# Kernel tuning notes

Hardware: AMD Instinct MI355X
Metric: run time of the kernel (lower is better)

## Reference

```python
import jax, jax.numpy as jnp
import numpy as np

LMAX = 8                         # lmax-1 used by s2/so3 irreps
DIMS = [2 * l + 1 for l in range(LMAX + 1)]
S2_OFF = np.cumsum([0] + DIMS).tolist()            # offsets into 81-dim s2 irreps
SO3_OFF = np.cumsum([0] + [d * d for d in DIMS]).tolist()  # offsets into 969-dim so3 irreps
S2_DIM = S2_OFF[-1]              # 81
SO3_DIM = SO3_OFF[-1]            # 969
F_IN = 81                        # multiplicity into S2Conv
F_SO3 = 300
C = 768                          # encoder feature channels
KS = 7                           # encoder feature map / kernel size
B = 8
G_S2 = 48                        # s2 healpix grid rec_level=1
G_ACT = 4096                     # SO3Activation grid points (stand-in for res=20 grid)
G_SO3 = 36864                    # so3 healpix grid rec_level=3


def setup_inputs() -> dict:
    key = jax.random.key(0)
    ks = jax.random.split(key, 7)
    return {
        "x": jax.random.normal(ks[0], (B, C, KS, KS), jnp.float32),
        "F": jax.random.normal(ks[1], (F_IN, S2_DIM * C, KS, KS), jnp.float32) * 0.02,
        "w_s2": jax.random.normal(ks[2], (F_IN, F_SO3, G_S2), jnp.float32) * 0.1,
        "Y": jax.random.normal(ks[3], (G_S2, S2_DIM), jnp.float32),
        "w_so3": jax.random.normal(ks[4], (F_SO3, 1, G_SO3), jnp.float32) * 0.1,
        "D": jax.random.normal(ks[5], (G_SO3, SO3_DIM), jnp.float32),
        "D_act": jax.random.normal(ks[6], (G_ACT, SO3_DIM), jnp.float32),
    }


def _forward(x, F, w_s2, Y, w_so3, D, D_act):
    b = x.shape[0]
    # ---- Induction layer: split expanded R2Conv filter into 768-channel chunks,
    # stack, contract with feature map. g_split: (n=81, c_out=81, C, 7, 7)
    g = jnp.swapaxes(F.reshape(F_IN, S2_DIM, C, KS, KS), 0, 1)
    y = jnp.einsum('ijkhw,akhw->aji', g, x)          # (B, 81, 81): (batch, f_in, s2 irreps)

    # ---- S2Conv: expand kernel into irrep space, per-l block linear (s2 -> so3 irreps)
    psi = jnp.einsum('ni,xyn->xyi', Y, w_s2) / np.sqrt(G_S2)  # (81, 300, 81)
    outs = []
    for l, d in enumerate(DIMS):
        o = S2_OFF[l]
        xl = y[:, :, o:o + d]                        # (B, f_in, 2l+1)
        wl = psi[:, :, o:o + d]                      # (f_in, f_out, mul_out=2l+1)
        ol = jnp.einsum('bfm,fgu->bgum', xl, wl) / np.sqrt(F_IN)
        outs.append(ol.reshape(b, F_SO3, d * d))
    z = jnp.concatenate(outs, axis=-1)               # (B, 300, 969)

    # ---- SO3Activation: to grid, relu, back to irreps
    s = jnp.einsum('bfi,gi->bfg', z, D_act)
    z = jnp.einsum('bfg,gi->bfi', jax.nn.relu(s), D_act) / G_ACT

    # ---- SO3Conv: expand kernel via Wigner-D buffer, per-l block linear (so3 -> so3)
    psi2 = jnp.einsum('ni,xyn->xyi', D, w_so3) / np.sqrt(G_SO3)  # (300, 1, 969)
    outs = []
    for l, d in enumerate(DIMS):
        o = SO3_OFF[l]
        xl = z[:, :, o:o + d * d].reshape(b, F_SO3, d, d)   # (B, f, u, m)
        wl = psi2[:, :, o:o + d * d].reshape(F_SO3, 1, d, d)  # (f, g, v, u)
        ol = jnp.einsum('bfum,fgvu->bgvm', xl, wl) / np.sqrt(F_SO3 * d)
        outs.append(ol.reshape(b, 1, d * d))
    return jnp.concatenate(outs, axis=-1)            # (B, 1, 969)


def reference(x, F, w_s2, Y, w_so3, D, D_act):
    return _forward(x, F, w_s2, Y, w_so3, D, D_act)
```

## Files before the change

kernel.cpp:

```cpp
#include <hip/hip_runtime.h>
#include <hip/hip_bf16.h>
#include <math.h>

#define THREADS 256

constexpr int B_    = 8;
constexpr int C_    = 768;
constexpr int KS_   = 7;
constexpr int F_IN  = 81;
constexpr int F_SO3 = 300;
constexpr int S2_DIM  = 81;
constexpr int SO3_DIM = 969;
constexpr int G_S2  = 48;
constexpr int G_ACT = 4096;
constexpr int G_SO3 = 36864;
constexpr int CKK   = C_ * KS_ * KS_;
constexpr int CKK4  = CKK / 4;
constexpr int NPAIR = F_IN * S2_DIM;

constexpr int D2_SPLIT = 4;
constexpr int E1_SPLIT = 16;
constexpr int F_SPLIT  = 5;

__constant__ int d_S2_OFF[10]  = {0, 1, 4, 9, 16, 25, 36, 49, 64, 81};
__constant__ int d_SO3_OFF[10] = {0, 1, 10, 35, 84, 165, 286, 455, 680, 969};

struct CEnt { unsigned char u, m, so, l; };
struct CLut { CEnt v[992]; };
constexpr CLut make_clut() {
  CLut t{};
  int S2O[10]  = {0, 1, 4, 9, 16, 25, 36, 49, 64, 81};
  int SO3O[10] = {0, 1, 10, 35, 84, 165, 286, 455, 680, 969};
  for (int i = 0; i < 969; ++i) {
    int l = 0;
    while (i >= SO3O[l + 1]) ++l;
    int d = 2 * l + 1, r = i - SO3O[l];
    t.v[i].u  = (unsigned char)(r / d);
    t.v[i].m  = (unsigned char)(r % d);
    t.v[i].so = (unsigned char)S2O[l];
    t.v[i].l  = (unsigned char)l;
  }
  return t;
}
__constant__ CLut g_clut = make_clut();

using short8 = __attribute__((ext_vector_type(8))) short;
using f32x4  = __attribute__((ext_vector_type(4))) float;
using f4v    = __attribute__((ext_vector_type(4))) float;

#define GL16(gp, lp)                                                        \
  __builtin_amdgcn_global_load_lds(                                         \
      (const __attribute__((address_space(1))) void*)(gp),                  \
      (__attribute__((address_space(3))) void*)(lp), 16, 0, 0)

#define WAIT_VMCNT6() asm volatile("s_waitcnt vmcnt(6)" ::: "memory")
#define BARRIER()                                   \
  do {                                              \
    __builtin_amdgcn_sched_barrier(0);              \
    __builtin_amdgcn_s_barrier();                   \
    __builtin_amdgcn_sched_barrier(0);              \
  } while (0)

constexpr size_t AL(size_t x) { return (x + 1023) & ~(size_t)1023; }
constexpr size_t O_Y     = 0;
constexpr size_t O_PSI   = O_Y     + AL((size_t)8 * NPAIR * 4);
constexpr size_t O_ZBF   = O_PSI   + AL((size_t)F_IN * F_SO3 * 81 * 4);
constexpr size_t O_DACT  = O_ZBF   + AL((size_t)2432 * 1024 * 2);
constexpr size_t O_DACTT = O_DACT  + AL((size_t)4096 * 1024 * 2);
constexpr size_t O_WSO3  = O_DACTT + AL((size_t)1024 * 4096 * 2);
constexpr size_t O_DT    = O_WSO3  + AL((size_t)384 * 36864 * 2);
constexpr size_t O_SBF   = O_DT    + AL((size_t)1024 * 36864 * 2);
constexpr size_t O_D2P   = O_SBF   + AL((size_t)2432 * 4096 * 2);
constexpr size_t O_E1P   = O_D2P   + AL((size_t)D2_SPLIT * 2432 * 1024 * 4);
constexpr size_t O_PSI2  = O_E1P   + AL((size_t)E1_SPLIT * 384 * 1024 * 4);
constexpr size_t O_SFP   = O_PSI2  + AL((size_t)F_SO3 * SO3_DIM * 4);
constexpr size_t FAST_NEED = O_SFP + AL((size_t)F_SPLIT * 8 * SO3_DIM * 4);

constexpr size_t WS_Y    = 0;
constexpr size_t WS_PSI  = 52488;
constexpr size_t WS_Z    = 2020788;
constexpr size_t WS_S    = 4346388;
constexpr size_t WS_Z2   = 14176788;
constexpr size_t WS_P2P  = 16502388;
constexpr size_t WS_PSI2 = 18827988;

__device__ __forceinline__ void stage_a_body(
    const float* __restrict__ Fm, const float* __restrict__ x, float* __restrict__ y,
    char* smemc, int blk) {
  const int p0  = blk * 3;
  const int tid = threadIdx.x;
  const f4v* __restrict__ F4 = (const f4v*)Fm;
  const f4v* __restrict__ x4 = (const f4v*)x;

  float acc[3][8];
#pragma unroll
  for (int p = 0; p < 3; ++p)
#pragma unroll
    for (int b = 0; b < 8; ++b) acc[p][b] = 0.f;

  for (int i = tid; i < CKK4; i += THREADS) {
    f4v xv[8];
#pragma unroll
    for (int b = 0; b < 8; ++b) xv[b] = x4[b * CKK4 + i];
#pragma unroll
    for (int p = 0; p < 3; ++p) {
      f4v fv = __builtin_nontemporal_load(&F4[(size_t)(p0 + p) * CKK4 + i]);
#pragma unroll
      for (int b = 0; b < 8; ++b)
        acc[p][b] += fv[0] * xv[b][0] + fv[1] * xv[b][1] + fv[2] * xv[b][2] + fv[3] * xv[b][3];
    }
  }

  float (*red)[24] = (float(*)[24])smemc;
  const int lane = tid & 63, wid = tid >> 6;
#pragma unroll
  for (int p = 0; p < 3; ++p) {
#pragma unroll
    for (int b = 0; b < 8; ++b) {
      float v = acc[p][b];
      v += __shfl_down(v, 32);
      v += __shfl_down(v, 16);
      v += __shfl_down(v, 8);
      v += __shfl_down(v, 4);
      v += __shfl_down(v, 2);
      v += __shfl_down(v, 1);
      if (lane == 0) red[wid][p * 8 + b] = v;
    }
  }
  __syncthreads();
  if (tid < 24) {
    float v = red[0][tid] + red[1][tid] + red[2][tid] + red[3][tid];
    int p = tid / 8, b = tid % 8;
    y[(size_t)b * NPAIR + p0 + p] = v;
  }
}

__global__ __launch_bounds__(THREADS) void k_stage_a3(
    const float* __restrict__ Fm, const float* __restrict__ x, float* __restrict__ y) {
  __shared__ __align__(16) char smem[512];
  stage_a_body(Fm, x, y, smem, blockIdx.x);
}

__device__ __forceinline__ void cvt4_body(const float* __restrict__ src,
                                          __hip_bfloat16* __restrict__ dst,
                                          int R, int Cs, int Cp, int blk) {
  size_t e0 = ((size_t)blk * THREADS + threadIdx.x) * 4;
  int r = (int)(e0 / (unsigned)Cp), c = (int)(e0 % (unsigned)Cp);
  __hip_bfloat16 o[4];
#pragma unroll
  for (int j = 0; j < 4; ++j) {
    float v = (r < R && c + j < Cs) ? src[(size_t)r * Cs + c + j] : 0.f;
    o[j] = __float2bfloat16(v);
  }
  *(ushort4*)(&dst[e0]) = *(const ushort4*)o;
}

__device__ __forceinline__ void tr_body(const float* __restrict__ src,
                                        __hip_bfloat16* __restrict__ dst,
                                        int R, int Cs, size_t dstStride, int bx, int by,
                                        char* smemc) {
  float (*tile)[33] = (float(*)[33])smemc;
  const int c0 = bx * 32, r0 = by * 32;
  const int tx = threadIdx.x & 31, ty = threadIdx.x >> 5;
#pragma unroll
  for (int i = 0; i < 32; i += 8) {
    int r = r0 + ty + i, c = c0 + tx;
    tile[ty + i][tx] = (c < Cs) ? src[(size_t)r * Cs + c] : 0.f;
  }
  __syncthreads();
  const int rp = threadIdx.x & 15;
  const int cl = threadIdx.x >> 4;
#pragma unroll
  for (int j = 0; j < 2; ++j) {
    int cc = cl + 16 * j;
    int c  = c0 + cc;
    if (c < Cs) {
      __hip_bfloat16 o[2];
      o[0] = __float2bfloat16(tile[2 * rp][cc]);
      o[1] = __float2bfloat16(tile[2 * rp + 1][cc]);
      *(ushort2*)(&dst[(size_t)c * dstStride + r0 + 2 * rp]) = *(const ushort2*)o;
    }
  }
}

__device__ __forceinline__ void psi_body(const float* __restrict__ w_s2,
                                         const float* __restrict__ Y,
                                         float* __restrict__ psi_t, int blk) {
  int idx = blk * THREADS + threadIdx.x;
  if (idx >= F_IN * F_SO3 * S2_DIM) return;
  int s  = idx % S2_DIM;
  int t1 = idx / S2_DIM;
  int f  = t1 % F_IN;
  int g  = t1 / F_IN;
  const float* w = w_s2 + ((size_t)f * F_SO3 + g) * G_S2;
  float acc = 0.f;
#pragma unroll 8
  for (int n = 0; n < G_S2; ++n) acc += w[n] * Y[n * S2_DIM + s];
  psi_t[idx] = acc * 0.14433756729740643f;
}

constexpr int UB1 = 4096;
constexpr int UB2 = 3968;
constexpr int UB3 = 13824;
constexpr int UB4 = 35712;
constexpr int UB5 = 7689;
constexpr int UB_TOT = UB1 + UB2 + UB3 + UB4 + UB5;

__global__ __launch_bounds__(THREADS) void k_uber(
    const float* __restrict__ D_act, __hip_bfloat16* __restrict__ Dact_bf,
    __hip_bfloat16* __restrict__ DactT_bf,
    const float* __restrict__ w_so3, __hip_bfloat16* __restrict__ wso3_bf,
    const float* __restrict__ D, __hip_bfloat16* __restrict__ DT_bf,
    const float* __restrict__ w_s2, const float* __restrict__ Y, float* __restrict__ psi_t) {
  __shared__ __align__(16) char smem[4352];
  int b = blockIdx.x;
  if (b < UB1) { cvt4_body(D_act, Dact_bf, G_ACT, SO3_DIM, 1024, b); return; }
  b -= UB1;
  if (b < UB2) { tr_body(D_act, DactT_bf, G_ACT, SO3_DIM, 4096, b % 31, b / 31, smem); return; }
  b -= UB2;
  if (b < UB3) { cvt4_body(w_so3, wso3_bf, F_SO3, G_SO3, G_SO3, b); return; }
  b -= UB3;
  if (b < UB4) { tr_body(D, DT_bf, G_SO3, SO3_DIM, 36864, b % 31, b / 31, smem); return; }
  b -= UB4;
  psi_body(w_s2, Y, psi_t, b);
}

__global__ __launch_bounds__(THREADS) void k_stage_c_bf(
    const float* __restrict__ y, const float* __restrict__ psi_t,
    __hip_bfloat16* __restrict__ z) {
  const int b = blockIdx.x / F_SO3;
  const int g = blockIdx.x % F_SO3;
  __shared__ float ybl[NPAIR];
  __shared__ float psl[NPAIR];
  const int tid = threadIdx.x;
  const float* pg = psi_t + (size_t)g * NPAIR;
  for (int t = tid; t < NPAIR; t += THREADS) {
    ybl[t] = y[(size_t)b * NPAIR + t];
    psl[t] = pg[t];
  }
  __syncthreads();
  for (int i = tid; i < 1024; i += THREADS) {
    float acc = 0.f;
    if (i < SO3_DIM) {
      CEnt e = g_clut.v[i];
      int im = e.so + e.m, iu = e.so + e.u;
#pragma unroll 9
      for (int f = 0; f < F_IN; ++f)
        acc += ybl[f * S2_DIM + im] * psl[f * S2_DIM + iu];
      acc *= (1.0f / 9.0f);
    }
    z[((size_t)b * F_SO3 + g) * 1024 + i] = __float2bfloat16(acc);
  }
}

struct G256 {
  const __hip_bfloat16* A;
  const __hip_bfloat16* B;
  void* C;
  int K, kSpan, Ncols;
  float scale;
  size_t splitStride;
  int gx, gy, gz, epi;
};

__device__ __forceinline__ void mfma256_body(const G256& g, unsigned lin, char* smem) {
  unsigned nwg = (unsigned)(g.gx * g.gy * g.gz);
  if ((nwg & 7u) == 0u) {
    unsigned q = nwg >> 3;
    lin = (lin & 7u) * q + (lin >> 3);
  }
  const int bxi = (int)(lin % (unsigned)g.gx);
  const unsigned t1 = lin / (unsigned)g.gx;
  const int byi = (int)(t1 % (unsigned)g.gy);
  const int bzi = (int)(t1 / (unsigned)g.gy);

  const int t    = threadIdx.x;
  const int lane = t & 63;
  const int wid  = t >> 6;
  const int wr   = wid >> 2, wc = wid & 3;
  const int bm = byi * 128, bn = bxi * 256;
  const int kBegin = bzi * g.kSpan;
  const int NG = g.kSpan >> 6;

  int aL[2], bL[4];
  const char* aSrc[2];
  const char* bSrc[4];
#pragma unroll
  for (int i = 0; i < 2; ++i) {
    int L = (i * 512 + t) * 16;
    int row = L >> 7;
    int kb  = (L & 127) ^ ((row & 7) << 4);
    aL[i] = L;
    aSrc[i] = (const char*)g.A + ((size_t)(bm + row) * g.K) * 2 + kb;
  }
#pragma unroll
  for (int i = 0; i < 4; ++i) {
    int L = (i * 512 + t) * 16;
    int row = L >> 7;
    int kb  = (L & 127) ^ ((row & 7) << 4);
    bL[i] = L;
    bSrc[i] = (const char*)g.B + ((size_t)(bn + row) * g.K) * 2 + kb;
  }

  auto STAGE = [&](int buf, int kt) {
    size_t ko = (size_t)(kBegin + (kt << 6)) * 2;
    char* Ab = smem + buf * 49152;
    char* Bb = Ab + 16384;
#pragma unroll
    for (int i = 0; i < 2; ++i) GL16(aSrc[i] + ko, Ab + aL[i]);
#pragma unroll
    for (int i = 0; i < 4; ++i) GL16(bSrc[i] + ko, Bb + bL[i]);
  };

  f32x4 acc[4][4] = {};

  STAGE(0, 0);
  STAGE(1, 1);
  WAIT_VMCNT6();
  BARRIER();

  int bi = 0;
  for (int gg = 0; gg < NG; ++gg) {
    char* Ab = smem + bi * 49152;
    char* Bb = Ab + 16384;
    short8 af[2][4], bf[2][4];

#pragma unroll
    for (int kk = 0; kk < 2; ++kk) {
      const int klin = (kk << 6) + ((lane >> 4) << 4);
#pragma unroll
      for (int m = 0; m < 4; ++m) {
        int ra = (wr << 6) + (m << 4) + (lane & 15);
        af[kk][m] = *(const short8*)(Ab + ra * 128 + (klin ^ ((ra & 7) << 4)));
      }
#pragma unroll
      for (int n = 0; n < 4; ++n) {
        int rb = (wc << 6) + (n << 4) + (lane & 15);
        bf[kk][n] = *(const short8*)(Bb + rb * 128 + (klin ^ ((rb & 7) << 4)));
      }
    }
    {
      int b2 = bi + 2; if (b2 >= 3) b2 -= 3;
      int kt2 = (gg + 2 < NG) ? gg + 2 : 0;
      STAGE(b2, kt2);
    }
    WAIT_VMCNT6();
    BARRIER();
    __builtin_amdgcn_s_setprio(1);
#pragma unroll
    for (int kk = 0; kk < 2; ++kk)
#pragma unroll
      for (int m = 0; m < 4; ++m)
#pragma unroll
        for (int n = 0; n < 4; ++n)
          acc[m][n] = __builtin_amdgcn_mfma_f32_16x16x32_bf16(af[kk][m], bf[kk][n], acc[m][n], 0, 0, 0);
    __builtin_amdgcn_s_setprio(0);
    BARRIER();

    if (++bi == 3) bi = 0;
  }

  const int rbase = bm + (wr << 6) + ((lane >> 4) << 2);
  const int cbase = bn + (wc << 6) + (lane & 15);
  if (g.epi == 0) {
    float* C = (float*)g.C + (size_t)bzi * g.splitStride;
#pragma unroll
    for (int m = 0; m < 4; ++m)
#pragma unroll
      for (int n = 0; n < 4; ++n)
#pragma unroll
        for (int r = 0; r < 4; ++r)
          C[(size_t)(rbase + m * 16 + r) * g.Ncols + (cbase + n * 16)] = acc[m][n][r] * g.scale;
  } else {
    __hip_bfloat16* C = (__hip_bfloat16*)g.C;
#pragma unroll
    for (int m = 0; m < 4; ++m)
#pragma unroll
      for (int n = 0; n < 4; ++n)
#pragma unroll
        for (int r = 0; r < 4; ++r)
          C[(size_t)(rbase + m * 16 + r) * g.Ncols + (cbase + n * 16)] =
              __float2bfloat16(fmaxf(acc[m][n][r], 0.f));
  }
}

__global__ __launch_bounds__(512) void k_g256_dual(G256 g0, G256 g1, int n0) {
  __shared__ __align__(16) char smem[147456];
  if ((int)blockIdx.x < n0) mfma256_body(g0, blockIdx.x, smem);
  else                      mfma256_body(g1, blockIdx.x - n0, smem);
}

__global__ __launch_bounds__(512) void k_g256_d2_e1r(
    G256 g, int n0,
    const float* __restrict__ parts, float* __restrict__ psi2) {
  __shared__ __align__(16) char smem[147456];
  if ((int)blockIdx.x < n0) { mfma256_body(g, blockIdx.x, smem); return; }
  int idx = (int)(blockIdx.x - n0) * 512 + threadIdx.x;
  if (idx >= F_SO3 * SO3_DIM) return;
  int r = idx / SO3_DIM, c = idx % SO3_DIM;
  float a = 0.f;
#pragma unroll
  for (int s = 0; s < E1_SPLIT; ++s) a += parts[(size_t)s * (384 * 1024) + (size_t)r * 1024 + c];
  psi2[(size_t)r * SO3_DIM + c] = a * (1.0f / 192.0f);
}

__global__ __launch_bounds__(THREADS) void k_stage_f_part(
    const float* __restrict__ d2p, const float* __restrict__ psi2, float* __restrict__ partial) {
  const int b  = blockIdx.x / 9;
  const int l  = blockIdx.x % 9;
  const int sp = blockIdx.y;
  const int d = 2 * l + 1, d2 = d * d;
  const int off = d_SO3_OFF[l];
  constexpr size_t SS = (size_t)2432 * 1024;
  __shared__ float zb[10][289];
  __shared__ float pb[10][289];
  const int tid = threadIdx.x;
  float acc[2] = {0.f, 0.f};
  const int fBeg = sp * (F_SO3 / F_SPLIT), fEnd = fBeg + F_SO3 / F_SPLIT;
  for (int fc = fBeg; fc < fEnd; fc += 10) {
    for (int t = tid; t < 10 * d2; t += THREADS) {
      int fl = t / d2, q = t - fl * d2;
      int f  = fc + fl;
      size_t zi = ((size_t)b * F_SO3 + f) * 1024 + off + q;
      float zv = 0.f;
#pragma unroll
      for (int s = 0; s < D2_SPLIT; ++s) zv += d2p[zi + (size_t)s * SS];
      zb[fl][q] = zv * (1.0f / G_ACT);
      pb[fl][q] = psi2[(size_t)f * SO3_DIM + off + q];
    }
    __syncthreads();
#pragma unroll 2
    for (int io = 0; io < 2; ++io) {
      int i = tid + io * THREADS;
      if (i < d2) {
        int v = i / d, m = i - v * d;
        float a = acc[io];
#pragma unroll
        for (int fl = 0; fl < 10; ++fl) {
          float s_ = 0.f;
          for (int u = 0; u < d; ++u)
            s_ += zb[fl][u * d + m] * pb[fl][v * d + u];
          a += s_;
        }
        acc[io] = a;
      }
    }
    __syncthreads();
  }
  for (int io = 0; io < 2; ++io) {
    int i = tid + io * THREADS;
    if (i < d2) partial[((size_t)sp * 8 + b) * SO3_DIM + off + i] = acc[io];
  }
}

__global__ __launch_bounds__(THREADS) void k_stage_f_red(
    const float* __restrict__ partial, float* __restrict__ out) {
  int idx = blockIdx.x * THREADS + threadIdx.x;
  if (idx >= 8 * SO3_DIM) return;
  int b = idx / SO3_DIM, i = idx % SO3_DIM;
  int l = g_clut.v[i].l;
  float a = 0.f;
#pragma unroll
  for (int sp = 0; sp < F_SPLIT; ++sp)
    a += partial[((size_t)sp * 8 + b) * SO3_DIM + i];
  out[(size_t)b * SO3_DIM + i] = a * rsqrtf(300.0f * (float)(2 * l + 1));
}

__global__ __launch_bounds__(THREADS) void k_psi(
    const float* __restrict__ w_s2, const float* __restrict__ Y, float* __restrict__ psi_t) {
  psi_body(w_s2, Y, psi_t, blockIdx.x);
}

__global__ __launch_bounds__(THREADS) void k_stage_c(
    const float* __restrict__ y, const float* __restrict__ psi_t, float* __restrict__ z) {
  const int b = blockIdx.x / F_SO3;
  const int g = blockIdx.x % F_SO3;
  __shared__ float ybl[NPAIR];
  __shared__ float psl[NPAIR];
  const int tid = threadIdx.x;
  const float* pg = psi_t + (size_t)g * NPAIR;
  for (int t = tid; t < NPAIR; t += THREADS) {
    ybl[t] = y[(size_t)b * NPAIR + t];
    psl[t] = pg[t];
  }
  __syncthreads();
  for (int i = tid; i < SO3_DIM; i += THREADS) {
    CEnt e = g_clut.v[i];
    int im = e.so + e.m, iu = e.so + e.u;
    float acc = 0.f;
#pragma unroll 9
    for (int f = 0; f < F_IN; ++f)
      acc += ybl[f * S2_DIM + im] * psl[f * S2_DIM + iu];
    z[((size_t)b * F_SO3 + g) * SO3_DIM + i] = acc * (1.0f / 9.0f);
  }
}

__global__ __launch_bounds__(THREADS) void k_gemm_nt_relu(
    const float* __restrict__ A, const float* __restrict__ Bm, float* __restrict__ Cm,
    int M, int N, int K) {
  __shared__ float As[16][68];
  __shared__ float Bs[16][68];
  const int bm = blockIdx.y * 64, bn = blockIdx.x * 64;
  const int t  = threadIdx.x;
  const int lk = t & 15, lm = t >> 4;
  const int tn = t & 15, tm = t >> 4;
  float acc[4][4] = {};
  for (int k0 = 0; k0 < K; k0 += 16) {
    int gk = k0 + lk;
#pragma unroll
    for (int j = 0; j < 4; ++j) {
      int m  = lm + 16 * j;
      int gm = bm + m;
      As[lk][m] = (gm < M && gk < K) ? A[(size_t)gm * K + gk] : 0.f;
      int gn = bn + m;
      Bs[lk][m] = (gn < N && gk < K) ? Bm[(size_t)gn * K + gk] : 0.f;
    }
    __syncthreads();
#pragma unroll
    for (int k = 0; k < 16; ++k) {
      float4 av = *(const float4*)&As[k][tm * 4];
      float4 bv = *(const float4*)&Bs[k][tn * 4];
      float a[4] = {av.x, av.y, av.z, av.w};
      float bb[4] = {bv.x, bv.y, bv.z, bv.w};
#pragma unroll
      for (int i2 = 0; i2 < 4; ++i2)
#pragma unroll
        for (int j2 = 0; j2 < 4; ++j2)
          acc[i2][j2] += a[i2] * bb[j2];
    }
    __syncthreads();
  }
#pragma unroll
  for (int i2 = 0; i2 < 4; ++i2) {
    int gm = bm + tm * 4 + i2;
    if (gm >= M) continue;
#pragma unroll
    for (int j2 = 0; j2 < 4; ++j2) {
      int gn = bn + tn * 4 + j2;
      if (gn < N) Cm[(size_t)gm * N + gn] = fmaxf(acc[i2][j2], 0.f);
    }
  }
}

__global__ __launch_bounds__(THREADS) void k_gemm_nn(
    const float* __restrict__ A, const float* __restrict__ Bm, float* __restrict__ Cm,
    int M, int N, int K, int kSpan, float scale, size_t cStride) {
  __shared__ float As[16][68];
  __shared__ float Bs[16][68];
  const int bm = blockIdx.y * 64, bn = blockIdx.x * 64;
  const int t   = threadIdx.x;
  const int lk  = t & 15, lm = t >> 4;
  const int ln  = t & 63, lkq = t >> 6;
  const int tn  = t & 15, tm = t >> 4;
  const int kBegin = blockIdx.z * kSpan;
  const int kEnd   = kBegin + kSpan;
  float* C = Cm + (size_t)blockIdx.z * cStride;
  float acc[4][4] = {};
  for (int k0 = kBegin; k0 < kEnd; k0 += 16) {
    {
      int gk = k0 + lk;
#pragma unroll
      for (int j = 0; j < 4; ++j) {
        int m = lm + 16 * j, gm = bm + m;
        As[lk][m] = (gm < M) ? A[(size_t)gm * K + gk] : 0.f;
      }
    }
    {
      int gn = bn + ln;
#pragma unroll
      for (int j = 0; j < 4; ++j) {
        int k = lkq + 4 * j;
        Bs[k][ln] = (gn < N) ? Bm[(size_t)(k0 + k) * N + gn] : 0.f;
      }
    }
    __syncthreads();
#pragma unroll
    for (int k = 0; k < 16; ++k) {
      float4 av = *(const float4*)&As[k][tm * 4];
      float4 bv = *(const float4*)&Bs[k][tn * 4];
      float a[4] = {av.x, av.y, av.z, av.w};
      float bb[4] = {bv.x, bv.y, bv.z, bv.w};
#pragma unroll
      for (int i2 = 0; i2 < 4; ++i2)
#pragma unroll
        for (int j2 = 0; j2 < 4; ++j2)
          acc[i2][j2] += a[i2] * bb[j2];
    }
    __syncthreads();
  }
#pragma unroll
  for (int i2 = 0; i2 < 4; ++i2) {
    int gm = bm + tm * 4 + i2;
    if (gm >= M) continue;
#pragma unroll
    for (int j2 = 0; j2 < 4; ++j2) {
      int gn = bn + tn * 4 + j2;
      if (gn < N) C[(size_t)gm * N + gn] = acc[i2][j2] * scale;
    }
  }
}

__global__ __launch_bounds__(THREADS) void k_reduce_psi2(
    const float* __restrict__ parts, float* __restrict__ psi2) {
  int idx = blockIdx.x * THREADS + threadIdx.x;
  if (idx >= F_SO3 * SO3_DIM) return;
  float acc = 0.f;
#pragma unroll
  for (int s = 0; s < 8; ++s) acc += parts[(size_t)s * (F_SO3 * SO3_DIM) + idx];
  psi2[idx] = acc * (1.0f / 192.0f);
}

__global__ __launch_bounds__(THREADS) void k_stage_f(
    const float* __restrict__ z2, const float* __restrict__ psi2, float* __restrict__ out,
    int zStride) {
  const int b = blockIdx.x / 9;
  const int l = blockIdx.x % 9;
  const int d = 2 * l + 1, d2 = d * d;
  const int off = d_SO3_OFF[l];
  __shared__ float zb[10][289];
  __shared__ float pb[10][289];
  const int tid = threadIdx.x;
  float acc[2] = {0.f, 0.f};
  const float scale = rsqrtf(300.0f * (float)d);
  for (int fc = 0; fc < F_SO3; fc += 10) {
    for (int t = tid; t < 10 * d2; t += THREADS) {
      int fl = t / d2, q = t - fl * d2;
      int f  = fc + fl;
      zb[fl][q] = z2[((size_t)b * F_SO3 + f) * zStride + off + q];
      pb[fl][q] = psi2[(size_t)f * SO3_DIM + off + q];
    }
    __syncthreads();
#pragma unroll 2
    for (int io = 0; io < 2; ++io) {
      int i = tid + io * THREADS;
      if (i < d2) {
        int v = i / d, m = i - v * d;
        float a = acc[io];
#pragma unroll
        for (int fl = 0; fl < 10; ++fl) {
          float s_ = 0.f;
          for (int u = 0; u < d; ++u)
            s_ += zb[fl][u * d + m] * pb[fl][v * d + u];
          a += s_;
        }
        acc[io] = a;
      }
    }
    __syncthreads();
  }
  for (int io = 0; io < 2; ++io) {
    int i = tid + io * THREADS;
    if (i < d2) out[(size_t)b * SO3_DIM + off + i] = acc[io] * scale;
  }
}

extern "C" void kernel_launch(void* const* d_in, const int* in_sizes, int n_in,
                              void* d_out, int out_size, void* d_ws, size_t ws_size,
                              hipStream_t stream) {
  const float* x     = (const float*)d_in[0];
  const float* Fm    = (const float*)d_in[1];
  const float* w_s2  = (const float*)d_in[2];
  const float* Y     = (const float*)d_in[3];
  const float* w_so3 = (const float*)d_in[4];
  const float* D     = (const float*)d_in[5];
  const float* D_act = (const float*)d_in[6];
  float* out = (float*)d_out;

  if (ws_size >= FAST_NEED) {
    char* p = (char*)d_ws;
    float*          y       = (float*)(p + O_Y);
    float*          psi     = (float*)(p + O_PSI);
    __hip_bfloat16* z_bf    = (__hip_bfloat16*)(p + O_ZBF);
    __hip_bfloat16* Dact_bf = (__hip_bfloat16*)(p + O_DACT);
    __hip_bfloat16* DactT_bf= (__hip_bfloat16*)(p + O_DACTT);
    __hip_bfloat16* wso3_bf = (__hip_bfloat16*)(p + O_WSO3);
    __hip_bfloat16* DT_bf   = (__hip_bfloat16*)(p + O_DT);
    __hip_bfloat16* s_bf    = (__hip_bfloat16*)(p + O_SBF);
    float*          d2p     = (float*)(p + O_D2P);
    float*          e1p     = (float*)(p + O_E1P);
    float*          psi2    = (float*)(p + O_PSI2);
    float*          sfp     = (float*)(p + O_SFP);

    k_stage_a3<<<NPAIR / 3, THREADS, 0, stream>>>(Fm, x, y);
    k_uber<<<UB_TOT, THREADS, 0, stream>>>(
        D_act, Dact_bf, DactT_bf, w_so3, wso3_bf, D, DT_bf, w_s2, Y, psi);
    k_stage_c_bf<<<B_ * F_SO3, THREADS, 0, stream>>>(y, psi, z_bf);

    G256 e1{wso3_bf, DT_bf, e1p, G_SO3, G_SO3 / E1_SPLIT, 1024, 1.f,
            (size_t)384 * 1024, 4, 3, E1_SPLIT, 0};
    G256 d1{z_bf, Dact_bf, s_bf, 1024, 1024, 4096, 1.f, 0, 16, 19, 1, 1};
    int nE1 = 4 * 3 * E1_SPLIT;
    int nD1 = 16 * 19;
    k_g256_dual<<<nE1 + nD1, 512, 0, stream>>>(e1, d1, nE1);

    G256 d2{s_bf, DactT_bf, d2p, 4096, 4096 / D2_SPLIT, 1024, 1.f,
            (size_t)2432 * 1024, 4, 19, D2_SPLIT, 0};
    int nD2  = 4 * 19 * D2_SPLIT;
    int nE1r = (F_SO3 * SO3_DIM + 511) / 512;
    k_g256_d2_e1r<<<nD2 + nE1r, 512, 0, stream>>>(d2, nD2, e1p, psi2);

    k_stage_f_part<<<dim3(B_ * 9, F_SPLIT), THREADS, 0, stream>>>(d2p, psi2, sfp);
    k_stage_f_red<<<(8 * SO3_DIM + THREADS - 1) / THREADS, THREADS, 0, stream>>>(sfp, out);
  } else {
    float* ws  = (float*)d_ws;
    float* y    = ws + WS_Y;
    float* psi  = ws + WS_PSI;
    float* z    = ws + WS_Z;
    float* s    = ws + WS_S;
    float* z2   = ws + WS_Z2;
    float* p2p  = ws + WS_P2P;
    float* psi2 = ws + WS_PSI2;

    k_stage_a3<<<NPAIR / 3, THREADS, 0, stream>>>(Fm, x, y);
    k_psi<<<(F_IN * F_SO3 * S2_DIM + THREADS - 1) / THREADS, THREADS, 0, stream>>>(w_s2, Y, psi);
    k_stage_c<<<B_ * F_SO3, THREADS, 0, stream>>>(y, psi, z);
    k_gemm_nt_relu<<<dim3(G_ACT / 64, (B_ * F_SO3 + 63) / 64), THREADS, 0, stream>>>(
        z, D_act, s, B_ * F_SO3, G_ACT, SO3_DIM);
    k_gemm_nn<<<dim3((SO3_DIM + 63) / 64, (B_ * F_SO3 + 63) / 64, 1), THREADS, 0, stream>>>(
        s, D_act, z2, B_ * F_SO3, SO3_DIM, G_ACT, G_ACT, 1.0f / G_ACT, 0);
    k_gemm_nn<<<dim3((SO3_DIM + 63) / 64, (F_SO3 + 63) / 64, 8), THREADS, 0, stream>>>(
        w_so3, D, p2p, F_SO3, SO3_DIM, G_SO3, G_SO3 / 8, 1.0f, (size_t)F_SO3 * SO3_DIM);
    k_reduce_psi2<<<(F_SO3 * SO3_DIM + THREADS - 1) / THREADS, THREADS, 0, stream>>>(p2p, psi2);
    k_stage_f<<<B_ * 9, THREADS, 0, stream>>>(z2, psi2, out, SO3_DIM);
  }
}
```

Before: 561.8 us.

## Stage MFMA epilogue through LDS for vector stores; register-block stage C

The GEMM epilogue now writes each wave's accumulator tile into a padded LDS staging area, then reads it back row-wise and issues 16-byte fp32 or 8-byte bf16 vector stores instead of scattered scalar stores. Separately, the S2Conv block-linear kernel is reorganized so each thread computes four consecutive m outputs for one (l,u) pair, reusing each psi value across four y reads, with padded LDS rows. This is meant to cut uncoalesced global writes and redundant LDS loads. It reuses the pipeline's shared memory for staging with no barrier before the overwrite, which could race with other waves, and the bf16 epilogue now multiplies by scale where it did not before.

```diff
diff --git a/kernel.cpp b/kernel.cpp
--- a/kernel.cpp
+++ b/kernel.cpp
@@ -43,6 +43,22 @@
   return t;
 }
 __constant__ CLut g_clut = make_clut();
+
+struct CItem { unsigned char l, u, m0; };
+struct CItems { CItem v[288]; };
+constexpr CItems make_citems() {
+  CItems t{};
+  int k = 0;
+  for (int l = 0; l < 9; ++l) {
+    int d = 2 * l + 1;
+    for (int u = 0; u < d; ++u)
+      for (int m0 = 0; m0 < d; m0 += 4)
+        t.v[k++] = {(unsigned char)l, (unsigned char)u, (unsigned char)m0};
+  }
+  return t;
+}
+__constant__ CItems g_citems = make_citems();
+constexpr int N_CITEMS = 285;
 
 using short8 = __attribute__((ext_vector_type(8))) short;
 using f32x4  = __attribute__((ext_vector_type(4))) float;
@@ -230,26 +246,48 @@
     __hip_bfloat16* __restrict__ z) {
   const int b = blockIdx.x / F_SO3;
   const int g = blockIdx.x % F_SO3;
-  __shared__ float ybl[NPAIR];
-  __shared__ float psl[NPAIR];
+  __shared__ float ybl[81 * 84];
+  __shared__ float psl[81 * 84];
   const int tid = threadIdx.x;
   const float* pg = psi_t + (size_t)g * NPAIR;
-  for (int t = tid; t < NPAIR; t += THREADS) {
-    ybl[t] = y[(size_t)b * NPAIR + t];
-    psl[t] = pg[t];
+  for (int idx = tid; idx < 81 * 84; idx += THREADS) {
+    int f = idx / 84, s = idx - f * 84;
+    float yv = 0.f, pv = 0.f;
+    if (s < 81) {
+      yv = y[(size_t)b * NPAIR + f * 81 + s];
+      pv = pg[f * 81 + s];
+    }
+    ybl[idx] = yv;
+    psl[idx] = pv;
   }
   __syncthreads();
-  for (int i = tid; i < 1024; i += THREADS) {
-    float acc = 0.f;
-    if (i < SO3_DIM) {
-      CEnt e = g_clut.v[i];
-      int im = e.so + e.m, iu = e.so + e.u;
-#pragma unroll 9
-      for (int f = 0; f < F_IN; ++f)
-        acc += ybl[f * S2_DIM + im] * psl[f * S2_DIM + iu];
-      acc *= (1.0f / 9.0f);
-    }
-    z[((size_t)b * F_SO3 + g) * 1024 + i] = __float2bfloat16(acc);
+
+  __hip_bfloat16* zrow = z + ((size_t)b * F_SO3 + g) * 1024;
+  if (tid < 1024 - 969) zrow[969 + tid] = __float2bfloat16(0.f);
+
+  for (int it = tid; it < N_CITEMS; it += THREADS) {
+    CItem e = g_citems.v[it];
+    const int d  = 2 * e.l + 1;
+    const int so = d_S2_OFF[e.l];
+    const int off = d_SO3_OFF[e.l];
+    const int base0 = so + e.m0;
+    const int pu = so + e.u;
+    float a0 = 0.f, a1 = 0.f, a2 = 0.f, a3 = 0.f;
+#pragma unroll 3
+    for (int f = 0; f < F_IN; ++f) {
+      const float* yb = &ybl[f * 84 + base0];
+      float pv = psl[f * 84 + pu];
+      a0 += pv * yb[0];
+      a1 += pv * yb[1];
+      a2 += pv * yb[2];
+      a3 += pv * yb[3];
+    }
+    int nm = d - e.m0;
+    size_t zo = (size_t)off + (size_t)e.u * d + e.m0;
+    zrow[zo] = __float2bfloat16(a0 * (1.0f / 9.0f));
+    if (nm > 1) zrow[zo + 1] = __float2bfloat16(a1 * (1.0f / 9.0f));
+    if (nm > 2) zrow[zo + 2] = __float2bfloat16(a2 * (1.0f / 9.0f));
+    if (nm > 3) zrow[zo + 3] = __float2bfloat16(a3 * (1.0f / 9.0f));
   }
 }
 
@@ -360,27 +398,39 @@
     if (++bi == 3) bi = 0;
   }
 
-  const int rbase = bm + (wr << 6) + ((lane >> 4) << 2);
-  const int cbase = bn + (wc << 6) + (lane & 15);
+  float* stg = (float*)(smem + wid * 17408);
+#pragma unroll
+  for (int m = 0; m < 4; ++m)
+#pragma unroll
+    for (int n = 0; n < 4; ++n)
+#pragma unroll
+      for (int r = 0; r < 4; ++r)
+        stg[(m * 16 + ((lane >> 4) << 2) + r) * 68 + n * 16 + (lane & 15)] = acc[m][n][r];
+
+  const int rowbase = bm + (wr << 6);
+  const int colbase = bn + (wc << 6);
   if (g.epi == 0) {
     float* C = (float*)g.C + (size_t)bzi * g.splitStride;
 #pragma unroll
-    for (int m = 0; m < 4; ++m)
-#pragma unroll
-      for (int n = 0; n < 4; ++n)
-#pragma unroll
-        for (int r = 0; r < 4; ++r)
-          C[(size_t)(rbase + m * 16 + r) * g.Ncols + (cbase + n * 16)] = acc[m][n][r] * g.scale;
+    for (int itv = 0; itv < 16; ++itv) {
+      int row  = itv * 4 + (lane >> 4);
+      int col4 = (lane & 15) * 4;
+      f4v v = *(const f4v*)&stg[row * 68 + col4];
+      f4v o = {v[0] * g.scale, v[1] * g.scale, v[2] * g.scale, v[3] * g.scale};
+      *(f4v*)&C[(size_t)(rowbase + row) * g.Ncols + colbase + col4] = o;
+    }
   } else {
     __hip_bfloat16* C = (__hip_bfloat16*)g.C;
 #pragma unroll
-    for (int m = 0; m < 4; ++m)
-#pragma unroll
-      for (int n = 0; n < 4; ++n)
-#pragma unroll
-        for (int r = 0; r < 4; ++r)
-          C[(size_t)(rbase + m * 16 + r) * g.Ncols + (cbase + n * 16)] =
-              __float2bfloat16(fmaxf(acc[m][n][r], 0.f));
+    for (int itv = 0; itv < 16; ++itv) {
+      int row  = itv * 4 + (lane >> 4);
+      int col4 = (lane & 15) * 4;
+      f4v v = *(const f4v*)&stg[row * 68 + col4];
+      __hip_bfloat16 o[4];
+#pragma unroll
+      for (int j = 0; j < 4; ++j) o[j] = __float2bfloat16(fmaxf(v[j] * g.scale, 0.f));
+      *(ushort4*)&C[(size_t)(rowbase + row) * g.Ncols + colbase + col4] = *(const ushort4*)o;
+    }
   }
 }
 
```

Result: slower. 594.2 us (+5.8%).

## Retile bf16 MFMA GEMMs to 128x128 tiles with 256-thread double buffering

Applied to the files above, without the earlier changes.

Replaces the 128x256, 512-thread, triple-buffered GEMM body with a 128x128 tile computed by 256 threads over two LDS buffers. Each buffer is refilled right after its fragments are read into registers, guarded by an lgkmcnt wait and a barrier. LDS per block drops from 144KB to 64KB, which should allow more resident blocks per CU, and the grids double in the N dimension. The K-split for the w_so3 x D GEMM rises from 16 to 24 to add more blocks, at the cost of more partial buffers to reduce. Smaller tiles lower data reuse per block, and the extra barrier per iteration adds synchronization.

```diff
diff --git a/kernel.cpp b/kernel.cpp
--- a/kernel.cpp
+++ b/kernel.cpp
@@ -19,7 +19,7 @@
 constexpr int NPAIR = F_IN * S2_DIM;
 
 constexpr int D2_SPLIT = 4;
-constexpr int E1_SPLIT = 16;
+constexpr int E1_SPLIT = 24;
 constexpr int F_SPLIT  = 5;
 
 __constant__ int d_S2_OFF[10]  = {0, 1, 4, 9, 16, 25, 36, 49, 64, 81};
@@ -53,7 +53,12 @@
       (const __attribute__((address_space(1))) void*)(gp),                  \
       (__attribute__((address_space(3))) void*)(lp), 16, 0, 0)
 
-#define WAIT_VMCNT6() asm volatile("s_waitcnt vmcnt(6)" ::: "memory")
+#define WAIT_VMCNT8() asm volatile("s_waitcnt vmcnt(8)" ::: "memory")
+#define LGKM0()                                     \
+  do {                                              \
+    asm volatile("s_waitcnt lgkmcnt(0)" ::: "memory"); \
+    __builtin_amdgcn_sched_barrier(0);              \
+  } while (0)
 #define BARRIER()                                   \
   do {                                              \
     __builtin_amdgcn_sched_barrier(0);              \
@@ -263,7 +268,7 @@
   int gx, gy, gz, epi;
 };
 
-__device__ __forceinline__ void mfma256_body(const G256& g, unsigned lin, char* smem) {
+__device__ __forceinline__ void mfma128_body(const G256& g, unsigned lin, char* smem) {
   unsigned nwg = (unsigned)(g.gx * g.gy * g.gz);
   if ((nwg & 7u) == 0u) {
     unsigned q = nwg >> 3;
@@ -277,37 +282,31 @@
   const int t    = threadIdx.x;
   const int lane = t & 63;
   const int wid  = t >> 6;
-  const int wr   = wid >> 2, wc = wid & 3;
-  const int bm = byi * 128, bn = bxi * 256;
+  const int wr   = wid >> 1, wc = wid & 1;
+  const int bm = byi * 128, bn = bxi * 128;
   const int kBegin = bzi * g.kSpan;
   const int NG = g.kSpan >> 6;
 
-  int aL[2], bL[4];
-  const char* aSrc[2];
+  int aL[4], bL[4];
+  const char* aSrc[4];
   const char* bSrc[4];
 #pragma unroll
-  for (int i = 0; i < 2; ++i) {
-    int L = (i * 512 + t) * 16;
+  for (int i = 0; i < 4; ++i) {
+    int L = (i * 256 + t) * 16;
     int row = L >> 7;
     int kb  = (L & 127) ^ ((row & 7) << 4);
     aL[i] = L;
     aSrc[i] = (const char*)g.A + ((size_t)(bm + row) * g.K) * 2 + kb;
-  }
-#pragma unroll
-  for (int i = 0; i < 4; ++i) {
-    int L = (i * 512 + t) * 16;
-    int row = L >> 7;
-    int kb  = (L & 127) ^ ((row & 7) << 4);
     bL[i] = L;
     bSrc[i] = (const char*)g.B + ((size_t)(bn + row) * g.K) * 2 + kb;
   }
 
   auto STAGE = [&](int buf, int kt) {
     size_t ko = (size_t)(kBegin + (kt << 6)) * 2;
-    char* Ab = smem + buf * 49152;
+    char* Ab = smem + buf * 32768;
     char* Bb = Ab + 16384;
 #pragma unroll
-    for (int i = 0; i < 2; ++i) GL16(aSrc[i] + ko, Ab + aL[i]);
+    for (int i = 0; i < 4; ++i) GL16(aSrc[i] + ko, Ab + aL[i]);
 #pragma unroll
     for (int i = 0; i < 4; ++i) GL16(bSrc[i] + ko, Bb + bL[i]);
   };
@@ -316,12 +315,12 @@
 
   STAGE(0, 0);
   STAGE(1, 1);
-  WAIT_VMCNT6();
+  WAIT_VMCNT8();
   BARRIER();
 
-  int bi = 0;
+  int cur = 0;
   for (int gg = 0; gg < NG; ++gg) {
-    char* Ab = smem + bi * 49152;
+    char* Ab = smem + cur * 32768;
     char* Bb = Ab + 16384;
     short8 af[2][4], bf[2][4];
 
@@ -339,12 +338,13 @@
         bf[kk][n] = *(const short8*)(Bb + rb * 128 + (klin ^ ((rb & 7) << 4)));
       }
     }
+    LGKM0();
+    BARRIER();
     {
-      int b2 = bi + 2; if (b2 >= 3) b2 -= 3;
       int kt2 = (gg + 2 < NG) ? gg + 2 : 0;
-      STAGE(b2, kt2);
-    }
-    WAIT_VMCNT6();
+      STAGE(cur, kt2);
+    }
+    WAIT_VMCNT8();
     BARRIER();
     __builtin_amdgcn_s_setprio(1);
 #pragma unroll
@@ -355,9 +355,8 @@
         for (int n = 0; n < 4; ++n)
           acc[m][n] = __builtin_amdgcn_mfma_f32_16x16x32_bf16(af[kk][m], bf[kk][n], acc[m][n], 0, 0, 0);
     __builtin_amdgcn_s_setprio(0);
-    BARRIER();
-
-    if (++bi == 3) bi = 0;
+
+    cur ^= 1;
   }
 
   const int rbase = bm + (wr << 6) + ((lane >> 4) << 2);
@@ -384,22 +383,22 @@
   }
 }
 
-__global__ __launch_bounds__(512) void k_g256_dual(G256 g0, G256 g1, int n0) {
-  __shared__ __align__(16) char smem[147456];
-  if ((int)blockIdx.x < n0) mfma256_body(g0, blockIdx.x, smem);
-  else                      mfma256_body(g1, blockIdx.x - n0, smem);
-}
-
-__global__ __launch_bounds__(512) void k_g256_d2_e1r(
+__global__ __launch_bounds__(THREADS) void k_g256_dual(G256 g0, G256 g1, int n0) {
+  __shared__ __align__(16) char smem[65536];
+  if ((int)blockIdx.x < n0) mfma128_body(g0, blockIdx.x, smem);
+  else                      mfma128_body(g1, blockIdx.x - n0, smem);
+}
+
+__global__ __launch_bounds__(THREADS) void k_g256_d2_e1r(
     G256 g, int n0,
     const float* __restrict__ parts, float* __restrict__ psi2) {
-  __shared__ __align__(16) char smem[147456];
-  if ((int)blockIdx.x < n0) { mfma256_body(g, blockIdx.x, smem); return; }
-  int idx = (int)(blockIdx.x - n0) * 512 + threadIdx.x;
+  __shared__ __align__(16) char smem[65536];
+  if ((int)blockIdx.x < n0) { mfma128_body(g, blockIdx.x, smem); return; }
+  int idx = (int)(blockIdx.x - n0) * THREADS + threadIdx.x;
   if (idx >= F_SO3 * SO3_DIM) return;
   int r = idx / SO3_DIM, c = idx % SO3_DIM;
   float a = 0.f;
-#pragma unroll
+#pragma unroll 8
   for (int s = 0; s < E1_SPLIT; ++s) a += parts[(size_t)s * (384 * 1024) + (size_t)r * 1024 + c];
   psi2[(size_t)r * SO3_DIM + c] = a * (1.0f / 192.0f);
 }
@@ -687,17 +686,17 @@
     k_stage_c_bf<<<B_ * F_SO3, THREADS, 0, stream>>>(y, psi, z_bf);
 
     G256 e1{wso3_bf, DT_bf, e1p, G_SO3, G_SO3 / E1_SPLIT, 1024, 1.f,
-            (size_t)384 * 1024, 4, 3, E1_SPLIT, 0};
-    G256 d1{z_bf, Dact_bf, s_bf, 1024, 1024, 4096, 1.f, 0, 16, 19, 1, 1};
-    int nE1 = 4 * 3 * E1_SPLIT;
-    int nD1 = 16 * 19;
-    k_g256_dual<<<nE1 + nD1, 512, 0, stream>>>(e1, d1, nE1);
+            (size_t)384 * 1024, 8, 3, E1_SPLIT, 0};
+    G256 d1{z_bf, Dact_bf, s_bf, 1024, 1024, 4096, 1.f, 0, 32, 19, 1, 1};
+    int nE1 = 8 * 3 * E1_SPLIT;
+    int nD1 = 32 * 19;
+    k_g256_dual<<<nE1 + nD1, THREADS, 0, stream>>>(e1, d1, nE1);
 
     G256 d2{s_bf, DactT_bf, d2p, 4096, 4096 / D2_SPLIT, 1024, 1.f,
-            (size_t)2432 * 1024, 4, 19, D2_SPLIT, 0};
-    int nD2  = 4 * 19 * D2_SPLIT;
-    int nE1r = (F_SO3 * SO3_DIM + 511) / 512;
-    k_g256_d2_e1r<<<nD2 + nE1r, 512, 0, stream>>>(d2, nD2, e1p, psi2);
+            (size_t)2432 * 1024, 8, 19, D2_SPLIT, 0};
+    int nD2  = 8 * 19 * D2_SPLIT;
+    int nE1r = (F_SO3 * SO3_DIM + THREADS - 1) / THREADS;
+    k_g256_d2_e1r<<<nD2 + nE1r, THREADS, 0, stream>>>(d2, nD2, e1p, psi2);
 
     k_stage_f_part<<<dim3(B_ * 9, F_SPLIT), THREADS, 0, stream>>>(d2p, psi2, sfp);
     k_stage_f_red<<<(8 * SO3_DIM + THREADS - 1) / THREADS, THREADS, 0, stream>>>(sfp, out);
```

Result: no change. 553.3 us (-1.5%).
